# Optimization experiments

Measured on AMD Instinct MI355X. Metric: run time of the kernel, lower is better.

## Reference

```python
import jax, jax.numpy as jnp
import numpy as np

DIM = 768
HEADS = 12
DIM_HEAD = DIM // HEADS  # 64
INNER = DIM_HEAD * HEADS  # 768
HIDDEN = 4 * DIM  # 3072
N = 31  # num_patches + 1, fixed by Block (num_patches=30)
B = 512
EPS = 1e-5
MASK_VAL = -987654321.0


def layernorm(x, g, b):
    mu = jnp.mean(x, axis=-1, keepdims=True)
    var = jnp.mean(jnp.square(x - mu), axis=-1, keepdims=True)
    return (x - mu) * jax.lax.rsqrt(var + EPS) * g + b


def setup_inputs() -> dict:
    key = jax.random.key(0)
    ks = jax.random.split(key, 12)
    s = 0.02
    return {
        "x": jax.random.normal(ks[0], (B, N, DIM), jnp.float32),
        "ln1_g": jnp.ones((DIM,), jnp.float32),
        "ln1_b": jnp.zeros((DIM,), jnp.float32),
        "w_qkv": jax.random.normal(ks[1], (DIM, 3 * INNER), jnp.float32) * s,
        "scale": jnp.full((HEADS,), DIM_HEAD ** -0.5, jnp.float32),
        "w_o": jax.random.normal(ks[2], (INNER, DIM), jnp.float32) * s,
        "b_o": jnp.zeros((DIM,), jnp.float32),
        "ln2_g": jnp.ones((DIM,), jnp.float32),
        "ln2_b": jnp.zeros((DIM,), jnp.float32),
        "w1": jax.random.normal(ks[3], (DIM, HIDDEN), jnp.float32) * s,
        "b1": jnp.zeros((HIDDEN,), jnp.float32),
        "w2": jax.random.normal(ks[4], (HIDDEN, DIM), jnp.float32) * s,
        "b2": jnp.zeros((DIM,), jnp.float32),
    }


def reference(x, ln1_g, ln1_b, w_qkv, scale, w_o, b_o, ln2_g, ln2_b, w1, b1, w2, b2):
    b, n, _ = x.shape
    # --- LSA attention ---
    h = layernorm(x, ln1_g, ln1_b)
    qkv = h @ w_qkv  # [b, n, 3*inner]
    q, k, v = jnp.split(qkv, 3, axis=-1)
    def split_heads(t):
        return t.reshape(b, n, HEADS, DIM_HEAD).transpose(0, 2, 1, 3)  # b h n d
    q, k, v = split_heads(q), split_heads(k), split_heads(v)
    dots = jnp.einsum('bhid,bhjd->bhij', q, k) * scale[None, :, None, None]
    # diagonal exclusion mask (self-token masked out)
    diag = jnp.eye(n, dtype=bool)
    dots = jnp.where(diag[None, None], MASK_VAL, dots)
    attn = jax.nn.softmax(dots, axis=-1)
    out = jnp.einsum('bhij,bhjd->bhid', attn, v)
    out = out.transpose(0, 2, 1, 3).reshape(b, n, INNER)
    x = x + out @ w_o + b_o
    # --- MLP ---
    h2 = layernorm(x, ln2_g, ln2_b)
    h2 = jax.nn.gelu(h2 @ w1 + b1, approximate=False)
    x = x + h2 @ w2 + b2
    return x
```

## Files before the change

### kernel.cpp

```cpp
#include <hip/hip_runtime.h>
#include <math.h>

#define DIM 768
#define HEADS 12
#define DHEAD 64
#define NTOK 31
#define BATCH 512
#define MTOK (BATCH * NTOK)
#define HIDDEN 3072
#define QKVN 2304
#define MASK_VAL -987654321.0f

typedef short s16x8 __attribute__((ext_vector_type(8)));
typedef float f32x4 __attribute__((ext_vector_type(4)));

static __device__ __forceinline__ float bs2f(unsigned short u) {
  unsigned int x = ((unsigned int)u) << 16;
  return __builtin_bit_cast(float, x);
}
static __device__ __forceinline__ unsigned short f2bs(float f) {
  unsigned int x = __builtin_bit_cast(unsigned int, f);
  x += 0x7fffu + ((x >> 16) & 1u);
  return (unsigned short)(x >> 16);
}

static __device__ __forceinline__ void gload16(const unsigned short* g, unsigned short* l) {
  __builtin_amdgcn_global_load_lds(
      (const __attribute__((address_space(1))) unsigned int*)g,
      (__attribute__((address_space(3))) unsigned int*)l, 16, 0, 0);
}

static __device__ __forceinline__ float epi_apply(int EPI, float v, int col, size_t idx,
                                                  const float* bias, const void* resid) {
  if (EPI == 0) return v;
  if (EPI == 2) {
    float t = v + bias[col];
    float arg = 1.5957691216f * t * (1.f + 0.044715f * t * t);
    return t * __builtin_amdgcn_rcpf(1.f + __expf(-arg));
  }
  if (EPI == 3) return v + bias[col] + ((const float*)resid)[idx];
  return v + bias[col] + bs2f(((const unsigned short*)resid)[idx]);
}

static __device__ __forceinline__ void epi_store(int EPI, void* outp, size_t idx, float t) {
  if (EPI == 4) ((float*)outp)[idx] = t;
  else ((unsigned short*)outp)[idx] = f2bs(t);
}

__global__ __launch_bounds__(256) void transpose_kernel(const float* __restrict__ w,
                                                        unsigned short* __restrict__ wt,
                                                        int K, int N) {
  __shared__ float t[64][65];
  int k0 = blockIdx.y * 64, n0 = blockIdx.x * 64;
  int tid = threadIdx.x;
  int r = tid >> 4, c4 = (tid & 15) * 4;
#pragma unroll
  for (int i = 0; i < 4; ++i) {
    float4 v = *(const float4*)(w + (size_t)(k0 + r + i * 16) * N + n0 + c4);
    t[r + i * 16][c4] = v.x;
    t[r + i * 16][c4 + 1] = v.y;
    t[r + i * 16][c4 + 2] = v.z;
    t[r + i * 16][c4 + 3] = v.w;
  }
  __syncthreads();
#pragma unroll
  for (int i = 0; i < 4; ++i) {
    int n = r + i * 16;
    ushort4 o;
    o.x = f2bs(t[c4 + 0][n]);
    o.y = f2bs(t[c4 + 1][n]);
    o.z = f2bs(t[c4 + 2][n]);
    o.w = f2bs(t[c4 + 3][n]);
    *(ushort4*)(wt + (size_t)(n0 + n) * K + k0 + c4) = o;
  }
}

__global__ __launch_bounds__(256) void ln_kernel(const float* __restrict__ x,
                                                 const float* __restrict__ g,
                                                 const float* __restrict__ bta,
                                                 unsigned short* __restrict__ out) {
  int wid = threadIdx.x >> 6, lane = threadIdx.x & 63;
  size_t row = (size_t)blockIdx.x * 4 + wid;
  const float4* xr = (const float4*)(x + row * DIM);
  float4 v[3];
  v[0] = xr[lane];
  v[1] = xr[lane + 64];
  v[2] = xr[lane + 128];
  float s = 0.f, sq = 0.f;
#pragma unroll
  for (int i = 0; i < 3; ++i) {
    s += v[i].x + v[i].y + v[i].z + v[i].w;
    sq += v[i].x * v[i].x + v[i].y * v[i].y + v[i].z * v[i].z + v[i].w * v[i].w;
  }
#pragma unroll
  for (int off = 32; off; off >>= 1) {
    s += __shfl_xor(s, off);
    sq += __shfl_xor(sq, off);
  }
  float mu = s * (1.f / DIM);
  float var = sq * (1.f / DIM) - mu * mu;
  float rs = rsqrtf(var + 1e-5f);
#pragma unroll
  for (int i = 0; i < 3; ++i) {
    int col = i * 256 + lane * 4;
    float4 gg = *(const float4*)(g + col);
    float4 bb = *(const float4*)(bta + col);
    ushort4 o;
    o.x = f2bs((v[i].x - mu) * rs * gg.x + bb.x);
    o.y = f2bs((v[i].y - mu) * rs * gg.y + bb.y);
    o.z = f2bs((v[i].z - mu) * rs * gg.z + bb.z);
    o.w = f2bs((v[i].w - mu) * rs * gg.w + bb.w);
    *(ushort4*)(out + row * DIM + col) = o;
  }
}

__global__ __launch_bounds__(256) void ln_bf16_kernel(const unsigned short* __restrict__ x,
                                                      const float* __restrict__ g,
                                                      const float* __restrict__ bta,
                                                      unsigned short* __restrict__ out) {
  int wid = threadIdx.x >> 6, lane = threadIdx.x & 63;
  size_t row = (size_t)blockIdx.x * 4 + wid;
  const unsigned short* xr = x + row * DIM;
  float v[12];
#pragma unroll
  for (int i = 0; i < 3; ++i) {
    ushort4 u = *(const ushort4*)(xr + i * 256 + lane * 4);
    v[i * 4 + 0] = bs2f(u.x);
    v[i * 4 + 1] = bs2f(u.y);
    v[i * 4 + 2] = bs2f(u.z);
    v[i * 4 + 3] = bs2f(u.w);
  }
  float s = 0.f, sq = 0.f;
#pragma unroll
  for (int i = 0; i < 12; ++i) {
    s += v[i];
    sq += v[i] * v[i];
  }
#pragma unroll
  for (int off = 32; off; off >>= 1) {
    s += __shfl_xor(s, off);
    sq += __shfl_xor(sq, off);
  }
  float mu = s * (1.f / DIM);
  float var = sq * (1.f / DIM) - mu * mu;
  float rs = rsqrtf(var + 1e-5f);
#pragma unroll
  for (int i = 0; i < 3; ++i) {
    int col = i * 256 + lane * 4;
    float4 gg = *(const float4*)(g + col);
    float4 bb = *(const float4*)(bta + col);
    ushort4 o;
    o.x = f2bs((v[i * 4 + 0] - mu) * rs * gg.x + bb.x);
    o.y = f2bs((v[i * 4 + 1] - mu) * rs * gg.y + bb.y);
    o.z = f2bs((v[i * 4 + 2] - mu) * rs * gg.z + bb.z);
    o.w = f2bs((v[i * 4 + 3] - mu) * rs * gg.w + bb.w);
    *(ushort4*)(out + row * DIM + col) = o;
  }
}

template <int BUF, int MH, int VM, typename STF>
__device__ __forceinline__ void gph128(const char* aP0, const char* bP0,
                                       s16x8 (&bk)[4], f32x4 (&acc)[4][4], STF&& stage) {
  const char* aP = aP0 + BUF * 8192 + MH * 2048;
  const char* bP = bP0 + BUF * 16384;
  s16x8 af[2];
  if (MH == 0) {
#pragma unroll
    for (int ni = 0; ni < 4; ++ni) bk[ni] = *(const s16x8*)(bP + ni * 1024);
  }
  af[0] = *(const s16x8*)(aP);
  af[1] = *(const s16x8*)(aP + 1024);
  stage();
  if (VM == 2) asm volatile("s_waitcnt vmcnt(2)");
  if (VM == 0) asm volatile("s_waitcnt vmcnt(0)");
  __builtin_amdgcn_s_barrier();
  asm volatile("s_waitcnt lgkmcnt(0)");
  __builtin_amdgcn_s_setprio(1);
#pragma unroll
  for (int mi = 0; mi < 2; ++mi)
#pragma unroll
    for (int ni = 0; ni < 4; ++ni)
      acc[MH * 2 + mi][ni] =
          __builtin_amdgcn_mfma_f32_16x16x32_bf16(af[mi], bk[ni], acc[MH * 2 + mi][ni], 0, 0, 0);
  __builtin_amdgcn_s_setprio(0);
  __builtin_amdgcn_s_barrier();
}

template <int EPI>
__device__ __forceinline__ void gemm128_body(
    const unsigned short* __restrict__ A, const unsigned short* __restrict__ Bt,
    void* __restrict__ outp, const float* __restrict__ bias,
    const void* __restrict__ resid, int M, int N, int K, int ntn) {
  __shared__ char ldsc[49152];
  int tid = threadIdx.x;
  int lane = tid & 63, w = tid >> 6;
  int wm = w >> 2, wn = w & 3;
  int fr = lane & 15, q = lane >> 4;

  int nwg = gridDim.x, orig = blockIdx.x;
  int qd = nwg >> 3, r8 = nwg & 7, xcd = orig & 7, loc = orig >> 3;
  int bid = (xcd < r8 ? xcd * (qd + 1) : r8 * (qd + 1) + (xcd - r8) * qd) + loc;
  int m0 = (bid / ntn) * 128, n0 = (bid % ntn) * 256;

  int rdoff = (q * 16) ^ (((fr >> 1) & 3) << 4);
  const char* aP0 = ldsc + (wm * 64 + fr) * 64 + rdoff;
  const char* bP0 = ldsc + 16384 + (wn * 64 + fr) * 64 + rdoff;

  int srow = tid >> 2;
  int seoff = (((tid & 3) ^ ((srow >> 1) & 3))) << 3;
  const char* Ab = (const char*)A + ((size_t)(m0 + srow) * K + seoff) * 2;
  const char* Bb = (const char*)Bt + ((size_t)(n0 + srow) * K + seoff) * 2;
  size_t rstep = (size_t)K * 256;

  auto stgA = [&](int buf, int tile) {
    gload16((const unsigned short*)(Ab + tile * 64),
            (unsigned short*)(ldsc + buf * 8192 + w * 1024));
  };
  auto stgB = [&](int buf, int tile) {
    const char* gp = Bb + tile * 64;
    char* lp = ldsc + 16384 + buf * 16384 + w * 1024;
    gload16((const unsigned short*)gp, (unsigned short*)lp);
    gload16((const unsigned short*)(gp + rstep), (unsigned short*)(lp + 8192));
  };
  auto nop = [&] {};

  f32x4 acc[4][4] = {};
  s16x8 bk[4];
  int NT = K / 32;

  stgA(0, 0);
  stgB(0, 0);
  stgB(1, 1);
  asm volatile("s_waitcnt vmcnt(2)");
  __builtin_amdgcn_s_barrier();

  for (int t = 0; t + 3 < NT; t += 2) {
    gph128<0, 0, -1>(aP0, bP0, bk, acc, [&] { stgA(1, t + 1); });
    gph128<0, 1, 2>(aP0, bP0, bk, acc, [&] { stgB(0, t + 2); });
    gph128<1, 0, -1>(aP0, bP0, bk, acc, [&] { stgA(0, t + 2); });
    gph128<1, 1, 2>(aP0, bP0, bk, acc, [&] { stgB(1, t + 3); });
  }
  gph128<0, 0, -1>(aP0, bP0, bk, acc, [&] { stgA(1, NT - 1); });
  gph128<0, 1, 0>(aP0, bP0, bk, acc, nop);
  gph128<1, 0, -1>(aP0, bP0, bk, acc, nop);
  gph128<1, 1, -1>(aP0, bP0, bk, acc, nop);

#pragma unroll
  for (int am = 0; am < 4; ++am)
#pragma unroll
    for (int ni = 0; ni < 4; ++ni)
#pragma unroll
      for (int rr = 0; rr < 4; ++rr) {
        int row = m0 + wm * 64 + am * 16 + q * 4 + rr;
        int col = n0 + wn * 64 + ni * 16 + fr;
        size_t idx = (size_t)row * N + col;
        epi_store(EPI, outp, idx, epi_apply(EPI, acc[am][ni][rr], col, idx, bias, resid));
      }
}

template <int BUF, int MH, int KH, int VM, typename STF>
__device__ __forceinline__ void gph192(const char* aB0, const char* bKH0, const char* bKH1,
                                       s16x8 (&bk)[3], f32x4 (&acc)[8][3], STF&& stage) {
  const char* aP = aB0 + BUF * 32768 + KH * 16384 + MH * 4096;
  s16x8 af[4];
  if (MH == 0) {
    const char* bp = (KH ? bKH1 : bKH0) + BUF * 24576;
#pragma unroll
    for (int ni = 0; ni < 3; ++ni) bk[ni] = *(const s16x8*)(bp + ni * 2048);
  }
#pragma unroll
  for (int mi = 0; mi < 4; ++mi) af[mi] = *(const s16x8*)(aP + mi * 1024);
  stage();
  if (VM == 2) asm volatile("s_waitcnt vmcnt(2)");
  if (VM == 0) asm volatile("s_waitcnt vmcnt(0)");
  __builtin_amdgcn_s_barrier();
  asm volatile("s_waitcnt lgkmcnt(0)");
  __builtin_amdgcn_s_setprio(1);
#pragma unroll
  for (int mi = 0; mi < 4; ++mi)
#pragma unroll
    for (int ni = 0; ni < 3; ++ni)
      acc[MH * 4 + mi][ni] =
          __builtin_amdgcn_mfma_f32_16x16x32_bf16(af[mi], bk[ni], acc[MH * 4 + mi][ni], 0, 0, 0);
  __builtin_amdgcn_s_setprio(0);
  __builtin_amdgcn_s_barrier();
}

template <int EPI>
__device__ __forceinline__ void gemm192_body(
    const unsigned short* __restrict__ A, const unsigned short* __restrict__ Bt,
    void* __restrict__ outp, const float* __restrict__ bias,
    const void* __restrict__ resid, int M, int N, int K, int ntn) {
  __shared__ char ldsc[114688];
  int tid = threadIdx.x;
  int lane = tid & 63, w = tid >> 6;
  int wm = w >> 2, wn = w & 3;
  int fr = lane & 15, q = lane >> 4;

  int nwg = gridDim.x, orig = blockIdx.x;
  int qd = nwg >> 3, r8 = nwg & 7, xcd = orig & 7, loc = orig >> 3;
  int bid = (xcd < r8 ? xcd * (qd + 1) : r8 * (qd + 1) + (xcd - r8) * qd) + loc;
  int m0 = (bid / ntn) * 256, n0 = (bid % ntn) * 192;

  int rdoffA = (q * 16) ^ (((fr >> 1) & 3) << 4);
  const char* aB0 = ldsc + (wm * 128 + fr) * 64 + rdoffA;
  int brow0 = wn * 48 + fr;
  int bsw = brow0 & 7;
  const char* bBase = ldsc + 65536 + brow0 * 128 + (q ^ (bsw & 3)) * 16;
  const char* bKH0 = bBase + ((0 ^ (bsw >> 2)) * 64);
  const char* bKH1 = bBase + ((1 ^ (bsw >> 2)) * 64);

  int srow = tid >> 2;
  int seoffA = (((tid & 3) ^ ((srow >> 1) & 3))) << 3;
  const char* Ab = (const char*)A + ((size_t)(m0 + srow) * K + seoffA) * 2;
  size_t rstep = (size_t)K * 256;
  auto stgA = [&](int kh, int buf, int tile) {
    const char* gp = Ab + tile * 128 + kh * 64;
    unsigned short* lp = (unsigned short*)(ldsc + buf * 32768 + kh * 16384 + w * 1024);
    gload16((const unsigned short*)gp, lp);
    gload16((const unsigned short*)(gp + rstep), (unsigned short*)((char*)lp + 8192));
  };
  const char* Bb2 = (const char*)Bt +
                    ((size_t)(n0 + (tid >> 3)) * K + (((tid & 7) ^ ((tid >> 3) & 7)) * 8)) * 2;
  auto stgB = [&](int j, int buf, int tile) {
    gload16((const unsigned short*)(Bb2 + (size_t)j * 128 * K + tile * 128),
            (unsigned short*)(ldsc + 65536 + buf * 24576 + j * 8192 + w * 1024));
  };
  auto nop = [&] {};

  f32x4 acc[8][3] = {};
  s16x8 bk[3];
  int NT = K / 64;

  stgA(0, 0, 0);
  stgA(1, 0, 0);
  stgB(0, 0, 0);
  stgB(1, 0, 0);
  stgB(2, 0, 0);
  stgA(0, 1, 1);
  asm volatile("s_waitcnt vmcnt(2)");
  __builtin_amdgcn_s_barrier();

  for (int t = 0; t + 3 < NT; t += 2) {
    gph192<0, 0, 0, -1>(aB0, bKH0, bKH1, bk, acc,
                        [&] { stgA(1, 1, t + 1); stgB(0, 1, t + 1); stgB(1, 1, t + 1); });
    gph192<0, 1, 0, -1>(aB0, bKH0, bKH1, bk, acc, [&] { stgB(2, 1, t + 1); });
    gph192<0, 0, 1, -1>(aB0, bKH0, bKH1, bk, acc, [&] { stgA(0, 0, t + 2); });
    gph192<0, 1, 1, 2>(aB0, bKH0, bKH1, bk, acc, nop);
    gph192<1, 0, 0, -1>(aB0, bKH0, bKH1, bk, acc,
                        [&] { stgA(1, 0, t + 2); stgB(0, 0, t + 2); stgB(1, 0, t + 2); });
    gph192<1, 1, 0, -1>(aB0, bKH0, bKH1, bk, acc, [&] { stgB(2, 0, t + 2); });
    gph192<1, 0, 1, -1>(aB0, bKH0, bKH1, bk, acc, [&] { stgA(0, 1, t + 3); });
    gph192<1, 1, 1, 2>(aB0, bKH0, bKH1, bk, acc, nop);
  }
  gph192<0, 0, 0, -1>(aB0, bKH0, bKH1, bk, acc,
                      [&] { stgA(1, 1, NT - 1); stgB(0, 1, NT - 1); stgB(1, 1, NT - 1); });
  gph192<0, 1, 0, -1>(aB0, bKH0, bKH1, bk, acc, [&] { stgB(2, 1, NT - 1); });
  gph192<0, 0, 1, -1>(aB0, bKH0, bKH1, bk, acc, nop);
  gph192<0, 1, 1, 0>(aB0, bKH0, bKH1, bk, acc, nop);
  gph192<1, 0, 0, -1>(aB0, bKH0, bKH1, bk, acc, nop);
  gph192<1, 1, 0, -1>(aB0, bKH0, bKH1, bk, acc, nop);
  gph192<1, 0, 1, -1>(aB0, bKH0, bKH1, bk, acc, nop);
  gph192<1, 1, 1, -1>(aB0, bKH0, bKH1, bk, acc, nop);

#pragma unroll
  for (int am = 0; am < 8; ++am)
#pragma unroll
    for (int ni = 0; ni < 3; ++ni)
#pragma unroll
      for (int rr = 0; rr < 4; ++rr) {
        int row = m0 + wm * 128 + am * 16 + q * 4 + rr;
        int col = n0 + wn * 48 + ni * 16 + fr;
        size_t idx = (size_t)row * N + col;
        epi_store(EPI, outp, idx, epi_apply(EPI, acc[am][ni][rr], col, idx, bias, resid));
      }
}

__global__ __launch_bounds__(512, 4) void gemm_qkv(const unsigned short* A,
                                                   const unsigned short* Bt, void* o,
                                                   const float* b, const void* r, int M,
                                                   int N, int K, int ntn) {
  gemm128_body<0>(A, Bt, o, b, r, M, N, K, ntn);
}
__global__ __launch_bounds__(512, 4) void gemm_mlp1(const unsigned short* A,
                                                    const unsigned short* Bt, void* o,
                                                    const float* b, const void* r, int M,
                                                    int N, int K, int ntn) {
  gemm128_body<2>(A, Bt, o, b, r, M, N, K, ntn);
}
__global__ __launch_bounds__(512, 2) void gemm_proj(const unsigned short* A,
                                                    const unsigned short* Bt, void* o,
                                                    const float* b, const void* r, int M,
                                                    int N, int K, int ntn) {
  gemm192_body<3>(A, Bt, o, b, r, M, N, K, ntn);
}
__global__ __launch_bounds__(512, 2) void gemm_mlp2(const unsigned short* A,
                                                    const unsigned short* Bt, void* o,
                                                    const float* b, const void* r, int M,
                                                    int N, int K, int ntn) {
  gemm192_body<4>(A, Bt, o, b, r, M, N, K, ntn);
}

__global__ __launch_bounds__(256) void attn_mfma_kernel(const unsigned short* __restrict__ qkv,
                                                        const float* __restrict__ scale,
                                                        unsigned short* __restrict__ ao) {
  __shared__ unsigned short Vt[4][64][40];
  __shared__ unsigned short Pl[4][32][32];
  int wid = threadIdx.x >> 6, lane = threadIdx.x & 63;
  int pair = blockIdx.x * 4 + wid;
  int b = pair / HEADS, h = pair % HEADS;
  const unsigned short* base = qkv + (size_t)b * NTOK * QKVN + h * DHEAD;
  const unsigned short* Qp = base;
  const unsigned short* Kp = base + 768;
  const unsigned short* Vp = base + 1536;

  int c = lane & 15, q = lane >> 4;
  int oct = q * 8;

  unsigned short vcol[NTOK];
#pragma unroll
  for (int j = 0; j < NTOK; ++j) vcol[j] = Vp[(size_t)j * QKVN + lane];
#pragma unroll
  for (int j = 0; j < NTOK; ++j) Vt[wid][lane][j] = vcol[j];
  Vt[wid][lane][31] = 0;

  s16x8 kf[2][2] = {{{0}}}, qf[2][2] = {{{0}}};
#pragma unroll
  for (int t = 0; t < 2; ++t) {
    int row = t * 16 + c;
    if (row < NTOK) {
#pragma unroll
      for (int s = 0; s < 2; ++s) {
        kf[t][s] = *(const s16x8*)(Kp + (size_t)row * QKVN + s * 32 + oct);
        qf[t][s] = *(const s16x8*)(Qp + (size_t)row * QKVN + s * 32 + oct);
      }
    }
  }

  f32x4 st[2][2] = {};
#pragma unroll
  for (int jt = 0; jt < 2; ++jt)
#pragma unroll
    for (int it = 0; it < 2; ++it)
#pragma unroll
      for (int s = 0; s < 2; ++s)
        st[jt][it] =
            __builtin_amdgcn_mfma_f32_16x16x32_bf16(kf[jt][s], qf[it][s], st[jt][it], 0, 0, 0);

  float scl = scale[h];
  float p[2][2][4];
#pragma unroll
  for (int it = 0; it < 2; ++it)
#pragma unroll
    for (int jt = 0; jt < 2; ++jt)
#pragma unroll
      for (int r = 0; r < 4; ++r) {
        int j = jt * 16 + 4 * q + r;
        int i = it * 16 + c;
        float v = st[jt][it][r] * scl;
        if (j == 31 || j == i) v = MASK_VAL;
        p[it][jt][r] = v;
      }
#pragma unroll
  for (int it = 0; it < 2; ++it) {
    float m = p[it][0][0];
#pragma unroll
    for (int jt = 0; jt < 2; ++jt)
#pragma unroll
      for (int r = 0; r < 4; ++r) m = fmaxf(m, p[it][jt][r]);
    m = fmaxf(m, __shfl_xor(m, 16));
    m = fmaxf(m, __shfl_xor(m, 32));
    float s = 0.f;
#pragma unroll
    for (int jt = 0; jt < 2; ++jt)
#pragma unroll
      for (int r = 0; r < 4; ++r) {
        float e = __expf(p[it][jt][r] - m);
        p[it][jt][r] = e;
        s += e;
      }
    s += __shfl_xor(s, 16);
    s += __shfl_xor(s, 32);
    float inv = __builtin_amdgcn_rcpf(s);
#pragma unroll
    for (int jt = 0; jt < 2; ++jt)
#pragma unroll
      for (int r = 0; r < 4; ++r) p[it][jt][r] *= inv;
  }
#pragma unroll
  for (int it = 0; it < 2; ++it)
#pragma unroll
    for (int jt = 0; jt < 2; ++jt) {
      unsigned int w0 =
          (unsigned int)f2bs(p[it][jt][0]) | ((unsigned int)f2bs(p[it][jt][1]) << 16);
      unsigned int w1 =
          (unsigned int)f2bs(p[it][jt][2]) | ((unsigned int)f2bs(p[it][jt][3]) << 16);
      uint2 pk = {w0, w1};
      *(uint2*)&Pl[wid][it * 16 + c][jt * 16 + 4 * q] = pk;
    }

  s16x8 pa[2];
#pragma unroll
  for (int it = 0; it < 2; ++it) pa[it] = *(const s16x8*)&Pl[wid][it * 16 + c][oct];
  f32x4 o[2][4];
#pragma unroll
  for (int it = 0; it < 2; ++it)
#pragma unroll
    for (int dt = 0; dt < 4; ++dt) {
      s16x8 vb = *(const s16x8*)&Vt[wid][dt * 16 + c][oct];
      f32x4 z = {0.f, 0.f, 0.f, 0.f};
      o[it][dt] = __builtin_amdgcn_mfma_f32_16x16x32_bf16(pa[it], vb, z, 0, 0, 0);
    }
#pragma unroll
  for (int it = 0; it < 2; ++it)
#pragma unroll
    for (int r = 0; r < 4; ++r) {
      int i = it * 16 + 4 * q + r;
      if (i < NTOK) {
        size_t rowoff = ((size_t)b * NTOK + i) * DIM + h * DHEAD;
#pragma unroll
        for (int dt = 0; dt < 4; ++dt) ao[rowoff + dt * 16 + c] = f2bs(o[it][dt][r]);
      }
    }
}

extern "C" void kernel_launch(void* const* d_in, const int* in_sizes, int n_in,
                              void* d_out, int out_size, void* d_ws, size_t ws_size,
                              hipStream_t stream) {
  (void)in_sizes; (void)n_in; (void)out_size; (void)ws_size;
  const float* x = (const float*)d_in[0];
  const float* ln1_g = (const float*)d_in[1];
  const float* ln1_b = (const float*)d_in[2];
  const float* w_qkv = (const float*)d_in[3];
  const float* scale = (const float*)d_in[4];
  const float* w_o = (const float*)d_in[5];
  const float* b_o = (const float*)d_in[6];
  const float* ln2_g = (const float*)d_in[7];
  const float* ln2_b = (const float*)d_in[8];
  const float* w1 = (const float*)d_in[9];
  const float* b1 = (const float*)d_in[10];
  const float* w2 = (const float*)d_in[11];
  const float* b2 = (const float*)d_in[12];

  char* ws = (char*)d_ws;
  unsigned short* buf1 = (unsigned short*)(ws + 0);
  unsigned short* qkv_bf = (unsigned short*)(ws + 24379392);
  unsigned short* x2 = (unsigned short*)(ws + 24379392);
  unsigned short* g_bf = (unsigned short*)(ws + 97517568);
  unsigned short* wqkvT = (unsigned short*)(ws + 195035136);
  unsigned short* woT = (unsigned short*)(ws + 198574080);
  unsigned short* w1T = (unsigned short*)(ws + 199753728);
  unsigned short* w2T = (unsigned short*)(ws + 204472320);

  transpose_kernel<<<dim3(QKVN / 64, DIM / 64), 256, 0, stream>>>(w_qkv, wqkvT, DIM, QKVN);
  transpose_kernel<<<dim3(DIM / 64, DIM / 64), 256, 0, stream>>>(w_o, woT, DIM, DIM);
  transpose_kernel<<<dim3(HIDDEN / 64, DIM / 64), 256, 0, stream>>>(w1, w1T, DIM, HIDDEN);
  transpose_kernel<<<dim3(DIM / 64, HIDDEN / 64), 256, 0, stream>>>(w2, w2T, HIDDEN, DIM);

  ln_kernel<<<MTOK / 4, 256, 0, stream>>>(x, ln1_g, ln1_b, buf1);
  gemm_qkv<<<(MTOK / 128) * (QKVN / 256), 512, 0, stream>>>(
      buf1, wqkvT, qkv_bf, nullptr, nullptr, MTOK, QKVN, DIM, QKVN / 256);
  attn_mfma_kernel<<<(BATCH * HEADS) / 4, 256, 0, stream>>>(qkv_bf, scale, buf1);
  gemm_proj<<<(MTOK / 256) * (DIM / 192), 512, 0, stream>>>(
      buf1, woT, x2, b_o, x, MTOK, DIM, DIM, DIM / 192);
  ln_bf16_kernel<<<MTOK / 4, 256, 0, stream>>>(x2, ln2_g, ln2_b, buf1);
  gemm_mlp1<<<(MTOK / 128) * (HIDDEN / 256), 512, 0, stream>>>(
      buf1, w1T, g_bf, b1, nullptr, MTOK, HIDDEN, DIM, HIDDEN / 256);
  gemm_mlp2<<<(MTOK / 256) * (DIM / 192), 512, 0, stream>>>(
      g_bf, w2T, (float*)d_out, b2, x2, MTOK, DIM, HIDDEN, DIM / 192);
}
```

Measured before the change: 322.7 us.

## Triple-buffer B tiles in the 128-row GEMM and merge the weight transposes

The 128x256 GEMM used for QKV and MLP1 now holds a third B buffer in LDS (64 KB instead of 48 KB). Each phase loads the full 4x4 fragment set and issues 16 MFMAs against one A/B buffer pair, with a fixed 24-k-tile schedule that rotates B across three slots and A across two. The goal is deeper prefetch with fewer barriers per MFMA, at the cost of more LDS per workgroup, which may lower occupancy, and a K hardcoded to 768. The four weight-transpose launches are also merged into one kernel that picks its matrix from the block index, saving launch overhead.

Result: no change. 323.7 us (+0.3%).

```diff
diff --git a/kernel.cpp b/kernel.cpp
--- a/kernel.cpp
+++ b/kernel.cpp
@@ -47,30 +47,41 @@
   else ((unsigned short*)outp)[idx] = f2bs(t);
 }
 
-__global__ __launch_bounds__(256) void transpose_kernel(const float* __restrict__ w,
-                                                        unsigned short* __restrict__ wt,
-                                                        int K, int N) {
-  __shared__ float t[64][65];
-  int k0 = blockIdx.y * 64, n0 = blockIdx.x * 64;
+__global__ __launch_bounds__(256) void transpose_all_kernel(
+    const float* __restrict__ w_qkv, const float* __restrict__ w_o,
+    const float* __restrict__ w1, const float* __restrict__ w2,
+    unsigned short* __restrict__ wqkvT, unsigned short* __restrict__ woT,
+    unsigned short* __restrict__ w1T, unsigned short* __restrict__ w2T) {
+  int t = blockIdx.x;
+  const float* w;
+  unsigned short* wt;
+  int K, N, tx;
+  if (t < 432) { w = w_qkv; wt = wqkvT; K = DIM; N = QKVN; tx = QKVN / 64; }
+  else if (t < 576) { t -= 432; w = w_o; wt = woT; K = DIM; N = DIM; tx = DIM / 64; }
+  else if (t < 1152) { t -= 576; w = w1; wt = w1T; K = DIM; N = HIDDEN; tx = HIDDEN / 64; }
+  else { t -= 1152; w = w2; wt = w2T; K = HIDDEN; N = DIM; tx = DIM / 64; }
+  int n0 = (t % tx) * 64, k0 = (t / tx) * 64;
+
+  __shared__ float tl[64][65];
   int tid = threadIdx.x;
   int r = tid >> 4, c4 = (tid & 15) * 4;
 #pragma unroll
   for (int i = 0; i < 4; ++i) {
     float4 v = *(const float4*)(w + (size_t)(k0 + r + i * 16) * N + n0 + c4);
-    t[r + i * 16][c4] = v.x;
-    t[r + i * 16][c4 + 1] = v.y;
-    t[r + i * 16][c4 + 2] = v.z;
-    t[r + i * 16][c4 + 3] = v.w;
+    tl[r + i * 16][c4] = v.x;
+    tl[r + i * 16][c4 + 1] = v.y;
+    tl[r + i * 16][c4 + 2] = v.z;
+    tl[r + i * 16][c4 + 3] = v.w;
   }
   __syncthreads();
 #pragma unroll
   for (int i = 0; i < 4; ++i) {
     int n = r + i * 16;
     ushort4 o;
-    o.x = f2bs(t[c4 + 0][n]);
-    o.y = f2bs(t[c4 + 1][n]);
-    o.z = f2bs(t[c4 + 2][n]);
-    o.w = f2bs(t[c4 + 3][n]);
+    o.x = f2bs(tl[c4 + 0][n]);
+    o.y = f2bs(tl[c4 + 1][n]);
+    o.z = f2bs(tl[c4 + 2][n]);
+    o.w = f2bs(tl[c4 + 3][n]);
     *(ushort4*)(wt + (size_t)(n0 + n) * K + k0 + c4) = o;
   }
 }
@@ -158,18 +169,16 @@
   }
 }
 
-template <int BUF, int MH, int VM, typename STF>
-__device__ __forceinline__ void gph128(const char* aP0, const char* bP0,
-                                       s16x8 (&bk)[4], f32x4 (&acc)[4][4], STF&& stage) {
-  const char* aP = aP0 + BUF * 8192 + MH * 2048;
-  const char* bP = bP0 + BUF * 16384;
-  s16x8 af[2];
-  if (MH == 0) {
-#pragma unroll
-    for (int ni = 0; ni < 4; ++ni) bk[ni] = *(const s16x8*)(bP + ni * 1024);
-  }
-  af[0] = *(const s16x8*)(aP);
-  af[1] = *(const s16x8*)(aP + 1024);
+template <int AB, int BB, int VM, typename STF>
+__device__ __forceinline__ void gphm(const char* aBase, const char* bBase,
+                                     f32x4 (&acc)[4][4], STF&& stage) {
+  const char* aP = aBase + AB * 8192;
+  const char* bP = bBase + BB * 16384;
+  s16x8 af[4], bk[4];
+#pragma unroll
+  for (int ni = 0; ni < 4; ++ni) bk[ni] = *(const s16x8*)(bP + ni * 1024);
+#pragma unroll
+  for (int mi = 0; mi < 4; ++mi) af[mi] = *(const s16x8*)(aP + mi * 1024);
   stage();
   if (VM == 2) asm volatile("s_waitcnt vmcnt(2)");
   if (VM == 0) asm volatile("s_waitcnt vmcnt(0)");
@@ -177,21 +186,21 @@
   asm volatile("s_waitcnt lgkmcnt(0)");
   __builtin_amdgcn_s_setprio(1);
 #pragma unroll
-  for (int mi = 0; mi < 2; ++mi)
+  for (int mi = 0; mi < 4; ++mi)
 #pragma unroll
     for (int ni = 0; ni < 4; ++ni)
-      acc[MH * 2 + mi][ni] =
-          __builtin_amdgcn_mfma_f32_16x16x32_bf16(af[mi], bk[ni], acc[MH * 2 + mi][ni], 0, 0, 0);
+      acc[mi][ni] =
+          __builtin_amdgcn_mfma_f32_16x16x32_bf16(af[mi], bk[ni], acc[mi][ni], 0, 0, 0);
   __builtin_amdgcn_s_setprio(0);
   __builtin_amdgcn_s_barrier();
 }
 
 template <int EPI>
-__device__ __forceinline__ void gemm128_body(
+__device__ __forceinline__ void gemm128m_body(
     const unsigned short* __restrict__ A, const unsigned short* __restrict__ Bt,
     void* __restrict__ outp, const float* __restrict__ bias,
     const void* __restrict__ resid, int M, int N, int K, int ntn) {
-  __shared__ char ldsc[49152];
+  __shared__ char ldsc[65536];
   int tid = threadIdx.x;
   int lane = tid & 63, w = tid >> 6;
   int wm = w >> 2, wn = w & 3;
@@ -203,8 +212,8 @@
   int m0 = (bid / ntn) * 128, n0 = (bid % ntn) * 256;
 
   int rdoff = (q * 16) ^ (((fr >> 1) & 3) << 4);
-  const char* aP0 = ldsc + (wm * 64 + fr) * 64 + rdoff;
-  const char* bP0 = ldsc + 16384 + (wn * 64 + fr) * 64 + rdoff;
+  const char* aBase = ldsc + (wm * 64 + fr) * 64 + rdoff;
+  const char* bBase = ldsc + 16384 + (wn * 64 + fr) * 64 + rdoff;
 
   int srow = tid >> 2;
   int seoff = (((tid & 3) ^ ((srow >> 1) & 3))) << 3;
@@ -225,25 +234,27 @@
   auto nop = [&] {};
 
   f32x4 acc[4][4] = {};
-  s16x8 bk[4];
-  int NT = K / 32;
-
   stgA(0, 0);
   stgB(0, 0);
   stgB(1, 1);
   asm volatile("s_waitcnt vmcnt(2)");
   __builtin_amdgcn_s_barrier();
 
-  for (int t = 0; t + 3 < NT; t += 2) {
-    gph128<0, 0, -1>(aP0, bP0, bk, acc, [&] { stgA(1, t + 1); });
-    gph128<0, 1, 2>(aP0, bP0, bk, acc, [&] { stgB(0, t + 2); });
-    gph128<1, 0, -1>(aP0, bP0, bk, acc, [&] { stgA(0, t + 2); });
-    gph128<1, 1, 2>(aP0, bP0, bk, acc, [&] { stgB(1, t + 3); });
-  }
-  gph128<0, 0, -1>(aP0, bP0, bk, acc, [&] { stgA(1, NT - 1); });
-  gph128<0, 1, 0>(aP0, bP0, bk, acc, nop);
-  gph128<1, 0, -1>(aP0, bP0, bk, acc, nop);
-  gph128<1, 1, -1>(aP0, bP0, bk, acc, nop);
+#pragma unroll 1
+  for (int T = 0; T < 18; T += 6) {
+    gphm<0, 0, 2>(aBase, bBase, acc, [&] { stgA(1, T + 1); stgB(2, T + 2); });
+    gphm<1, 1, 2>(aBase, bBase, acc, [&] { stgA(0, T + 2); stgB(0, T + 3); });
+    gphm<0, 2, 2>(aBase, bBase, acc, [&] { stgA(1, T + 3); stgB(1, T + 4); });
+    gphm<1, 0, 2>(aBase, bBase, acc, [&] { stgA(0, T + 4); stgB(2, T + 5); });
+    gphm<0, 1, 2>(aBase, bBase, acc, [&] { stgA(1, T + 5); stgB(0, T + 6); });
+    gphm<1, 2, 2>(aBase, bBase, acc, [&] { stgA(0, T + 6); stgB(1, T + 7); });
+  }
+  gphm<0, 0, 2>(aBase, bBase, acc, [&] { stgA(1, 19); stgB(2, 20); });
+  gphm<1, 1, 2>(aBase, bBase, acc, [&] { stgA(0, 20); stgB(0, 21); });
+  gphm<0, 2, 2>(aBase, bBase, acc, [&] { stgA(1, 21); stgB(1, 22); });
+  gphm<1, 0, 2>(aBase, bBase, acc, [&] { stgA(0, 22); stgB(2, 23); });
+  gphm<0, 1, 0>(aBase, bBase, acc, [&] { stgA(1, 23); });
+  gphm<1, 2, -1>(aBase, bBase, acc, nop);
 
 #pragma unroll
   for (int am = 0; am < 4; ++am)
@@ -380,13 +391,13 @@
                                                    const unsigned short* Bt, void* o,
                                                    const float* b, const void* r, int M,
                                                    int N, int K, int ntn) {
-  gemm128_body<0>(A, Bt, o, b, r, M, N, K, ntn);
+  gemm128m_body<0>(A, Bt, o, b, r, M, N, K, ntn);
 }
 __global__ __launch_bounds__(512, 4) void gemm_mlp1(const unsigned short* A,
                                                     const unsigned short* Bt, void* o,
                                                     const float* b, const void* r, int M,
                                                     int N, int K, int ntn) {
-  gemm128_body<2>(A, Bt, o, b, r, M, N, K, ntn);
+  gemm128m_body<2>(A, Bt, o, b, r, M, N, K, ntn);
 }
 __global__ __launch_bounds__(512, 2) void gemm_proj(const unsigned short* A,
                                                     const unsigned short* Bt, void* o,
@@ -552,10 +563,7 @@
   unsigned short* w1T = (unsigned short*)(ws + 199753728);
   unsigned short* w2T = (unsigned short*)(ws + 204472320);
 
-  transpose_kernel<<<dim3(QKVN / 64, DIM / 64), 256, 0, stream>>>(w_qkv, wqkvT, DIM, QKVN);
-  transpose_kernel<<<dim3(DIM / 64, DIM / 64), 256, 0, stream>>>(w_o, woT, DIM, DIM);
-  transpose_kernel<<<dim3(HIDDEN / 64, DIM / 64), 256, 0, stream>>>(w1, w1T, DIM, HIDDEN);
-  transpose_kernel<<<dim3(DIM / 64, HIDDEN / 64), 256, 0, stream>>>(w2, w2T, HIDDEN, DIM);
+  transpose_all_kernel<<<1728, 256, 0, stream>>>(w_qkv, w_o, w1, w2, wqkvT, woT, w1T, w2T);
 
   ln_kernel<<<MTOK / 4, 256, 0, stream>>>(x, ln1_g, ln1_b, buf1);
   gemm_qkv<<<(MTOK / 128) * (QKVN / 256), 512, 0, stream>>>(
```
